# Kernel optimization log

Hardware: AMD Instinct MI355X
Metric: run time of the kernel (lower is better)

Reference implementation:

```python
import jax, jax.numpy as jnp
import numpy as np

B, T, C = 4, 2048, 1024
H = 16
HD = C // H  # 64


def setup_inputs() -> dict:
    key = jax.random.key(0)
    k1, k2, k3 = jax.random.split(key, 3)
    x = jax.random.normal(k1, (B, T, C), dtype=jnp.float32)
    # learned params (torch Linear y = x @ W.T stored here as [in, out])
    Wqkv = jax.random.normal(k2, (C, 3 * C), dtype=jnp.float32) * (C ** -0.5)
    Wout = jax.random.normal(k3, (C, C), dtype=jnp.float32) * (C ** -0.5)
    bout = jnp.zeros((C,), dtype=jnp.float32)
    causal_mask = jnp.tril(jnp.ones((1, 1, T, T), dtype=bool))
    return {"x": x, "causal_mask": causal_mask, "Wqkv": Wqkv, "Wout": Wout, "bout": bout}


def reference(x, causal_mask, Wqkv, Wout, bout):
    b, t, c = x.shape
    scale = HD ** -0.5
    qkv = x @ Wqkv  # [B,T,3C]
    q, k, v = jnp.split(qkv, 3, axis=-1)
    # [B,T,C] -> [B,H,T,hd]
    q = q.reshape(b, t, H, HD).transpose(0, 2, 1, 3)
    k = k.reshape(b, t, H, HD).transpose(0, 2, 1, 3)
    v = v.reshape(b, t, H, HD).transpose(0, 2, 1, 3)
    att = jnp.einsum("bhqd,bhkd->bhqk", q, k) * scale  # [B,H,T,T]
    att = jnp.where(causal_mask, att, -jnp.inf)
    att = jax.nn.softmax(att, axis=-1)
    # dropout in eval mode == identity
    out = jnp.einsum("bhqk,bhkd->bhqd", att, v)  # [B,H,T,hd]
    out = out.transpose(0, 2, 1, 3).reshape(b, t, c)
    return out @ Wout + bout


if __name__ == "__main__":
    inp = setup_inputs()
    y = jax.jit(reference)(**inp)
    print(y.shape, y.dtype)
```

## Files before the change

kernel.cpp:

```cpp
#include <hip/hip_runtime.h>
#include <hip/hip_bf16.h>
#include <stdint.h>


typedef __bf16 bf16;
typedef __bf16 bf16x4 __attribute__((ext_vector_type(4)));
typedef __bf16 bf16x8 __attribute__((ext_vector_type(8)));
typedef float floatx4 __attribute__((ext_vector_type(4)));

#define MFMA16(a, b, c) __builtin_amdgcn_mfma_f32_16x16x32_bf16(a, b, c, 0, 0, 0)

#if defined(__has_builtin)
#if __has_builtin(__builtin_amdgcn_global_load_lds)
#define HAS_GLL 1
#endif
#endif

#ifdef HAS_GLL
__device__ __forceinline__ void gll16(const bf16* g, bf16* l) {
  __builtin_amdgcn_global_load_lds(
      (const __attribute__((address_space(1))) unsigned int*)g,
      (__attribute__((address_space(3))) unsigned int*)l, 16, 0, 0);
}
#endif

__global__ __launch_bounds__(256)
void convert_x(const float* __restrict__ in, bf16* __restrict__ out) {
  const size_t i = (size_t)blockIdx.x * 256 + threadIdx.x;
  const float4* p = (const float4*)in + i * 2;
  float4 a = p[0], b = p[1];
  bf16x8 v;
  v[0] = (bf16)a.x; v[1] = (bf16)a.y; v[2] = (bf16)a.z; v[3] = (bf16)a.w;
  v[4] = (bf16)b.x; v[5] = (bf16)b.y; v[6] = (bf16)b.z; v[7] = (bf16)b.w;
  *((bf16x8*)out + i) = v;
}

__global__ __launch_bounds__(256)
void transpose_w(const float* __restrict__ W, bf16* __restrict__ Wt, int K, int N) {
  __shared__ bf16 tile[32][33];
  const int k0 = blockIdx.y * 32, n0 = blockIdx.x * 32;
  const int t = threadIdx.x;
  {
    const int r = t >> 3, c4 = (t & 7) * 4;
    float4 v = *(const float4*)(W + (size_t)(k0 + r) * N + n0 + c4);
    tile[r][c4 + 0] = (bf16)v.x;
    tile[r][c4 + 1] = (bf16)v.y;
    tile[r][c4 + 2] = (bf16)v.z;
    tile[r][c4 + 3] = (bf16)v.w;
  }
  __syncthreads();
  {
    const int nr = t >> 3, kc = (t & 7) * 4;
    bf16x4 o;
#pragma unroll
    for (int j = 0; j < 4; ++j) o[j] = tile[kc + j][nr];
    *(bf16x4*)(Wt + (size_t)(n0 + nr) * K + k0 + kc) = o;
  }
}

template <int MODE>
__global__ __launch_bounds__(256, 3)
void gemm_bt(const bf16* __restrict__ A, const bf16* __restrict__ Bt,
             const float* __restrict__ bias, void* __restrict__ Cv,
             bf16* __restrict__ Vout, int M, int N, int K) {
  __shared__ __align__(16) bf16 As[128 * 64];
  __shared__ __align__(16) bf16 Bs[128 * 64];

  const int t = threadIdx.x, lane = t & 63, w = t >> 6;
  const int m_ = lane & 15, quad = lane >> 4;
  const int wm = w >> 1, wn = w & 1;
  const int m0 = blockIdx.y * 128, n0 = blockIdx.x * 128;

  floatx4 acc[4][4];
#pragma unroll
  for (int i = 0; i < 4; ++i)
#pragma unroll
    for (int j = 0; j < 4; ++j) {
      floatx4 z = {0.f, 0.f, 0.f, 0.f};
      acc[i][j] = z;
    }

  for (int k0 = 0; k0 < K; k0 += 64) {
#pragma unroll
    for (int i = 0; i < 4; ++i) {
      const int R0 = i * 32 + w * 8;
      const int R = R0 + (lane >> 3);
      const int sg = (lane & 7) ^ (R & 7);
      const bf16* ga = A + (size_t)(m0 + R) * K + k0 + sg * 8;
      const bf16* gb = Bt + (size_t)(n0 + R) * K + k0 + sg * 8;
#ifdef HAS_GLL
      gll16(ga, As + (size_t)R0 * 64);
      gll16(gb, Bs + (size_t)R0 * 64);
#else
      *(bf16x8*)(As + (size_t)R * 64 + (lane & 7) * 8) = *(const bf16x8*)ga;
      *(bf16x8*)(Bs + (size_t)R * 64 + (lane & 7) * 8) = *(const bf16x8*)gb;
#endif
    }
    __syncthreads();

#pragma unroll
    for (int kc = 0; kc < 2; ++kc) {
      bf16x8 af[4], bfr[4];
#pragma unroll
      for (int mt = 0; mt < 4; ++mt) {
        const int r = wm * 64 + mt * 16 + m_;
        const int slot = ((kc << 2) | quad) ^ (r & 7);
        af[mt] = *(const bf16x8*)(As + (size_t)r * 64 + slot * 8);
      }
#pragma unroll
      for (int nt = 0; nt < 4; ++nt) {
        const int rn = wn * 64 + nt * 16 + m_;
        const int slot = ((kc << 2) | quad) ^ (rn & 7);
        bfr[nt] = *(const bf16x8*)(Bs + (size_t)rn * 64 + slot * 8);
      }
#pragma unroll
      for (int mt = 0; mt < 4; ++mt)
#pragma unroll
        for (int nt = 0; nt < 4; ++nt)
          acc[mt][nt] = MFMA16(af[mt], bfr[nt], acc[mt][nt]);
    }
    __syncthreads();
  }

  if (MODE == 0) {
#pragma unroll
    for (int mt = 0; mt < 4; ++mt)
#pragma unroll
      for (int nt = 0; nt < 4; ++nt) {
        const int col = n0 + wn * 64 + nt * 16 + m_;
        const float bv = bias[col];
#pragma unroll
        for (int r = 0; r < 4; ++r) {
          const int row = m0 + wm * 64 + mt * 16 + quad * 4 + r;
          ((float*)Cv)[(size_t)row * N + col] = acc[mt][nt][r] + bv;
        }
      }
  } else {
    if (n0 < 2048) {
      const float sc = (n0 < 1024) ? 0.18033688f : 1.0f;
#pragma unroll
      for (int mt = 0; mt < 4; ++mt)
#pragma unroll
        for (int nt = 0; nt < 4; ++nt) {
          const int col = n0 + wn * 64 + nt * 16 + m_;
#pragma unroll
          for (int r = 0; r < 4; ++r) {
            const int row = m0 + wm * 64 + mt * 16 + quad * 4 + r;
            ((bf16*)Cv)[(size_t)row * 2048 + col] = (bf16)(acc[mt][nt][r] * sc);
          }
        }
    } else {
#pragma unroll
      for (int mt = 0; mt < 4; ++mt) {
        const int rowb = m0 + wm * 64 + mt * 16 + quad * 4;
        const int bb = rowb >> 11, tok = rowb & 2047;
#pragma unroll
        for (int nt = 0; nt < 4; ++nt) {
          const int c = n0 - 2048 + wn * 64 + nt * 16 + m_;
          const int h = c >> 6, d = c & 63;
          bf16x4 pw;
#pragma unroll
          for (int r = 0; r < 4; ++r) pw[r] = (bf16)acc[mt][nt][r];
          *(bf16x4*)(Vout + ((size_t)(bb * 16 + h) * 64 + d) * 2048 + tok) = pw;
        }
      }
    }
  }
}

__global__ __launch_bounds__(256, 2)
void attn_fwd(const bf16* __restrict__ qk, const bf16* __restrict__ vtp,
              bf16* __restrict__ attnout) {
  constexpr int KS = 72;
  __shared__ __align__(16) bf16 Ks[64 * KS];
  __shared__ __align__(16) bf16 VT[64 * KS];
  __shared__ __align__(16) bf16 Pl[128 * KS];

  const int t = threadIdx.x, lane = t & 63, w = t >> 6;
  const int m_ = lane & 15, quad = lane >> 4;
  const int bh = blockIdx.x;
  const int qbmap[16] = {15, 14, 13, 12, 8, 9, 10, 11, 7, 6, 5, 4, 0, 1, 2, 3};
  const int qb = qbmap[blockIdx.y];
  const int b = bh >> 4, h = bh & 15;
  const int srcbase = (lane & 48) + ((lane & 48) >> 2);

  const bf16* Qp = qk + (size_t)b * 2048 * 2048 + h * 64;
  const bf16* Kp = qk + (size_t)b * 2048 * 2048 + 1024 + h * 64;
  const bf16* Vt = vtp + (size_t)bh * 64 * 2048;

  const int sr0 = t >> 3, sg0 = t & 7;
  const int sr1 = (t + 256) >> 3, sg1 = t & 7;

  const int q0w = qb * 128 + w * 32;

  bf16x8 qf[2][2];
#pragma unroll
  for (int mt = 0; mt < 2; ++mt)
#pragma unroll
    for (int kc = 0; kc < 2; ++kc)
      qf[mt][kc] = *(const bf16x8*)(Qp + (size_t)(q0w + mt * 16 + m_) * 2048 +
                                    kc * 32 + quad * 8);

  floatx4 o[2][4];
#pragma unroll
  for (int mt = 0; mt < 2; ++mt)
#pragma unroll
    for (int nt = 0; nt < 4; ++nt) {
      floatx4 z = {0.f, 0.f, 0.f, 0.f};
      o[mt][nt] = z;
    }
  float lrow[2] = {0.f, 0.f};

  const int nch = 2 * qb + 2;

  bf16x8 kr0, kr1, vr0, vr1;
  kr0 = *(const bf16x8*)(Kp + (size_t)sr0 * 2048 + sg0 * 8);
  kr1 = *(const bf16x8*)(Kp + (size_t)sr1 * 2048 + sg1 * 8);
  vr0 = *(const bf16x8*)(Vt + (size_t)sr0 * 2048 + sg0 * 8);
  vr1 = *(const bf16x8*)(Vt + (size_t)sr1 * 2048 + sg1 * 8);

  for (int ch = 0; ch < nch; ++ch) {
    const int kb = ch * 64;
    __syncthreads();
    *(bf16x8*)(Ks + (size_t)sr0 * KS + sg0 * 8) = kr0;
    *(bf16x8*)(Ks + (size_t)sr1 * KS + sg1 * 8) = kr1;
    *(bf16x8*)(VT + (size_t)sr0 * KS + sg0 * 8) = vr0;
    *(bf16x8*)(VT + (size_t)sr1 * KS + sg1 * 8) = vr1;
    __syncthreads();
    if (ch + 1 < nch) {
      const int kn = kb + 64;
      kr0 = *(const bf16x8*)(Kp + (size_t)(kn + sr0) * 2048 + sg0 * 8);
      kr1 = *(const bf16x8*)(Kp + (size_t)(kn + sr1) * 2048 + sg1 * 8);
      vr0 = *(const bf16x8*)(Vt + (size_t)sr0 * 2048 + kn + sg0 * 8);
      vr1 = *(const bf16x8*)(Vt + (size_t)sr1 * 2048 + kn + sg1 * 8);
    }

    if (kb <= q0w + 31) {
      bf16x8 kf[4][2];
#pragma unroll
      for (int kt = 0; kt < 4; ++kt)
#pragma unroll
        for (int kc = 0; kc < 2; ++kc)
          kf[kt][kc] = *(const bf16x8*)(Ks + (size_t)(kt * 16 + m_) * KS +
                                        kc * 32 + quad * 8);
      const bool need_mask = (kb + 63 > q0w);
#pragma unroll
      for (int mt = 0; mt < 2; ++mt) {
        floatx4 s[4];
#pragma unroll
        for (int kt = 0; kt < 4; ++kt) {
          floatx4 z = {0.f, 0.f, 0.f, 0.f};
          z = MFMA16(kf[kt][0], qf[mt][0], z);
          z = MFMA16(kf[kt][1], qf[mt][1], z);
          s[kt] = z;
        }
        if (need_mask) {
          const int qglob = q0w + mt * 16 + m_;
#pragma unroll
          for (int kt = 0; kt < 4; ++kt)
#pragma unroll
            for (int r = 0; r < 4; ++r)
              if (kb + kt * 16 + quad * 4 + r > qglob) s[kt][r] = -1e30f;
        }
        float psum = 0.f;
#pragma unroll
        for (int kt = 0; kt < 4; ++kt) {
          bf16x4 pw;
#pragma unroll
          for (int r = 0; r < 4; ++r) {
            const float p = exp2f(s[kt][r]);
            psum += p;
            pw[r] = (bf16)p;
          }
          *(bf16x4*)(Pl + (size_t)((w * 2 + mt) * 16 + m_) * KS + kt * 16 +
                     quad * 4) = pw;
        }
        lrow[mt] += psum;
      }
      bf16x8 vf[4][2];
#pragma unroll
      for (int nt = 0; nt < 4; ++nt)
#pragma unroll
        for (int kc = 0; kc < 2; ++kc)
          vf[nt][kc] = *(const bf16x8*)(VT + (size_t)(nt * 16 + m_) * KS +
                                        kc * 32 + quad * 8);
#pragma unroll
      for (int mt = 0; mt < 2; ++mt) {
        const bf16* prow = Pl + (size_t)((w * 2 + mt) * 16 + m_) * KS;
        const bf16x8 pf0 = *(const bf16x8*)(prow + quad * 8);
        const bf16x8 pf1 = *(const bf16x8*)(prow + 32 + quad * 8);
#pragma unroll
        for (int nt = 0; nt < 4; ++nt) {
          o[mt][nt] = MFMA16(pf0, vf[nt][0], o[mt][nt]);
          o[mt][nt] = MFMA16(pf1, vf[nt][1], o[mt][nt]);
        }
      }
    }
  }

#pragma unroll
  for (int mt = 0; mt < 2; ++mt) {
    float l = lrow[mt];
    l += __shfl_xor(l, 16);
    l += __shfl_xor(l, 32);
    const float linv = 1.0f / l;
#pragma unroll
    for (int r = 0; r < 4; ++r) {
      const float inv = __shfl(linv, srcbase + r);
      const int row = q0w + mt * 16 + quad * 4 + r;
      const size_t orow = ((size_t)b * 2048 + row) * 1024 + h * 64;
#pragma unroll
      for (int nt = 0; nt < 4; ++nt)
        attnout[orow + nt * 16 + m_] = (bf16)(o[mt][nt][r] * inv);
    }
  }
}

extern "C" void kernel_launch(void* const* d_in, const int* in_sizes, int n_in,
                              void* d_out, int out_size, void* d_ws, size_t ws_size,
                              hipStream_t stream) {
  (void)in_sizes; (void)n_in; (void)out_size; (void)ws_size;
  const float* x    = (const float*)d_in[0];
  const float* Wqkv = (const float*)d_in[2];
  const float* Wout = (const float*)d_in[3];
  const float* bout = (const float*)d_in[4];
  float* out = (float*)d_out;

  bf16* qk      = (bf16*)d_ws;
  bf16* vtp     = (bf16*)((char*)d_ws + (size_t)32 * 1024 * 1024);
  bf16* attnout = (bf16*)((char*)d_ws + (size_t)48 * 1024 * 1024);
  bf16* Wout_t  = (bf16*)d_ws;
  bf16* xbf    = (bf16*)d_out;
  bf16* Wqkv_t = (bf16*)d_out + (size_t)8192 * 1024;

  convert_x<<<4096, 256, 0, stream>>>(x, xbf);
  transpose_w<<<dim3(96, 32), 256, 0, stream>>>(Wqkv, Wqkv_t, 1024, 3072);

  gemm_bt<1><<<dim3(24, 64), 256, 0, stream>>>(xbf, Wqkv_t, nullptr, qk, vtp,
                                               8192, 3072, 1024);
  attn_fwd<<<dim3(64, 16), 256, 0, stream>>>(qk, vtp, attnout);

  transpose_w<<<dim3(32, 32), 256, 0, stream>>>(Wout, Wout_t, 1024, 1024);
  gemm_bt<0><<<dim3(8, 64), 256, 0, stream>>>(attnout, Wout_t, bout, out,
                                              nullptr, 8192, 1024, 1024);
}
```

Before: 265.1 us.

## Rewrite attention inner loop with 32x32 MFMA, register-resident P, and double-buffered LDS

```diff
diff --git a/kernel.cpp b/kernel.cpp
--- a/kernel.cpp
+++ b/kernel.cpp
@@ -7,8 +7,11 @@
 typedef __bf16 bf16x4 __attribute__((ext_vector_type(4)));
 typedef __bf16 bf16x8 __attribute__((ext_vector_type(8)));
 typedef float floatx4 __attribute__((ext_vector_type(4)));
+typedef float floatx16 __attribute__((ext_vector_type(16)));
+typedef unsigned int uintx4 __attribute__((ext_vector_type(4)));
 
 #define MFMA16(a, b, c) __builtin_amdgcn_mfma_f32_16x16x32_bf16(a, b, c, 0, 0, 0)
+#define MFMA32(a, b, c) __builtin_amdgcn_mfma_f32_32x32x16_bf16(a, b, c, 0, 0, 0)
 
 #if defined(__has_builtin)
 #if __has_builtin(__builtin_amdgcn_global_load_lds)
@@ -23,6 +26,15 @@
       (__attribute__((address_space(3))) unsigned int*)l, 16, 0, 0);
 }
 #endif
+
+__device__ __forceinline__ unsigned cvtpk(float lo, float hi) {
+  unsigned r;
+  asm("v_cvt_pk_bf16_f32 %0, %1, %2" : "=v"(r) : "v"(lo), "v"(hi));
+  return r;
+}
+__device__ __forceinline__ void pl32swap(unsigned& a, unsigned& b) {
+  asm volatile("v_permlane32_swap_b32 %0, %1" : "+v"(a), "+v"(b));
+}
 
 __global__ __launch_bounds__(256)
 void convert_x(const float* __restrict__ in, bf16* __restrict__ out) {
@@ -168,150 +180,145 @@
   }
 }
 
+__device__ __forceinline__ void stage64(const bf16* base, bf16* lds,
+                                        int lane, int w) {
+#pragma unroll
+  for (int i = 0; i < 2; ++i) {
+    const int seg = w * 2 + i;
+    const int row = seg * 8 + (lane >> 3);
+    const int g = (lane & 7) ^ (row & 7);
+#ifdef HAS_GLL
+    gll16(base + (size_t)row * 2048 + g * 8, lds + seg * 512);
+#else
+    *(bf16x8*)(lds + row * 64 + (lane & 7) * 8) =
+        *(const bf16x8*)(base + (size_t)row * 2048 + g * 8);
+#endif
+  }
+}
+
 __global__ __launch_bounds__(256, 2)
 void attn_fwd(const bf16* __restrict__ qk, const bf16* __restrict__ vtp,
               bf16* __restrict__ attnout) {
-  constexpr int KS = 72;
-  __shared__ __align__(16) bf16 Ks[64 * KS];
-  __shared__ __align__(16) bf16 VT[64 * KS];
-  __shared__ __align__(16) bf16 Pl[128 * KS];
+  __shared__ __align__(16) bf16 KsB[2][64 * 64];
+  __shared__ __align__(16) bf16 VTB[2][64 * 64];
+  __shared__ __align__(16) float Lbuf[4][32];
 
   const int t = threadIdx.x, lane = t & 63, w = t >> 6;
-  const int m_ = lane & 15, quad = lane >> 4;
+  const int ln = lane & 31, hi = lane >> 5;
   const int bh = blockIdx.x;
   const int qbmap[16] = {15, 14, 13, 12, 8, 9, 10, 11, 7, 6, 5, 4, 0, 1, 2, 3};
   const int qb = qbmap[blockIdx.y];
   const int b = bh >> 4, h = bh & 15;
-  const int srcbase = (lane & 48) + ((lane & 48) >> 2);
 
   const bf16* Qp = qk + (size_t)b * 2048 * 2048 + h * 64;
   const bf16* Kp = qk + (size_t)b * 2048 * 2048 + 1024 + h * 64;
   const bf16* Vt = vtp + (size_t)bh * 64 * 2048;
 
-  const int sr0 = t >> 3, sg0 = t & 7;
-  const int sr1 = (t + 256) >> 3, sg1 = t & 7;
-
   const int q0w = qb * 128 + w * 32;
 
-  bf16x8 qf[2][2];
-#pragma unroll
-  for (int mt = 0; mt < 2; ++mt)
-#pragma unroll
-    for (int kc = 0; kc < 2; ++kc)
-      qf[mt][kc] = *(const bf16x8*)(Qp + (size_t)(q0w + mt * 16 + m_) * 2048 +
-                                    kc * 32 + quad * 8);
-
-  floatx4 o[2][4];
-#pragma unroll
-  for (int mt = 0; mt < 2; ++mt)
-#pragma unroll
-    for (int nt = 0; nt < 4; ++nt) {
-      floatx4 z = {0.f, 0.f, 0.f, 0.f};
-      o[mt][nt] = z;
-    }
-  float lrow[2] = {0.f, 0.f};
+  bf16x8 qf[4];
+#pragma unroll
+  for (int st = 0; st < 4; ++st)
+    qf[st] = *(const bf16x8*)(Qp + (size_t)(q0w + ln) * 2048 + st * 16 + hi * 8);
+
+  floatx16 o[2];
+#pragma unroll
+  for (int nt = 0; nt < 2; ++nt)
+#pragma unroll
+    for (int r = 0; r < 16; ++r) o[nt][r] = 0.f;
+  float lrow = 0.f;
 
   const int nch = 2 * qb + 2;
 
-  bf16x8 kr0, kr1, vr0, vr1;
-  kr0 = *(const bf16x8*)(Kp + (size_t)sr0 * 2048 + sg0 * 8);
-  kr1 = *(const bf16x8*)(Kp + (size_t)sr1 * 2048 + sg1 * 8);
-  vr0 = *(const bf16x8*)(Vt + (size_t)sr0 * 2048 + sg0 * 8);
-  vr1 = *(const bf16x8*)(Vt + (size_t)sr1 * 2048 + sg1 * 8);
+  stage64(Kp, KsB[0], lane, w);
+  stage64(Vt, VTB[0], lane, w);
 
   for (int ch = 0; ch < nch; ++ch) {
     const int kb = ch * 64;
-    __syncthreads();
-    *(bf16x8*)(Ks + (size_t)sr0 * KS + sg0 * 8) = kr0;
-    *(bf16x8*)(Ks + (size_t)sr1 * KS + sg1 * 8) = kr1;
-    *(bf16x8*)(VT + (size_t)sr0 * KS + sg0 * 8) = vr0;
-    *(bf16x8*)(VT + (size_t)sr1 * KS + sg1 * 8) = vr1;
+    const int cur = ch & 1;
     __syncthreads();
     if (ch + 1 < nch) {
-      const int kn = kb + 64;
-      kr0 = *(const bf16x8*)(Kp + (size_t)(kn + sr0) * 2048 + sg0 * 8);
-      kr1 = *(const bf16x8*)(Kp + (size_t)(kn + sr1) * 2048 + sg1 * 8);
-      vr0 = *(const bf16x8*)(Vt + (size_t)sr0 * 2048 + kn + sg0 * 8);
-      vr1 = *(const bf16x8*)(Vt + (size_t)sr1 * 2048 + kn + sg1 * 8);
-    }
-
-    if (kb <= q0w + 31) {
-      bf16x8 kf[4][2];
-#pragma unroll
-      for (int kt = 0; kt < 4; ++kt)
-#pragma unroll
-        for (int kc = 0; kc < 2; ++kc)
-          kf[kt][kc] = *(const bf16x8*)(Ks + (size_t)(kt * 16 + m_) * KS +
-                                        kc * 32 + quad * 8);
-      const bool need_mask = (kb + 63 > q0w);
-#pragma unroll
-      for (int mt = 0; mt < 2; ++mt) {
-        floatx4 s[4];
-#pragma unroll
-        for (int kt = 0; kt < 4; ++kt) {
-          floatx4 z = {0.f, 0.f, 0.f, 0.f};
-          z = MFMA16(kf[kt][0], qf[mt][0], z);
-          z = MFMA16(kf[kt][1], qf[mt][1], z);
-          s[kt] = z;
-        }
+      stage64(Kp + (size_t)(kb + 64) * 2048, KsB[cur ^ 1], lane, w);
+      stage64(Vt + kb + 64, VTB[cur ^ 1], lane, w);
+    }
+    if (kb > q0w + 31) continue;
+    const bf16* Kb = KsB[cur];
+    const bf16* Vb = VTB[cur];
+    const bool need_mask = (kb + 63 > q0w);
+
+#pragma unroll
+    for (int kt = 0; kt < 2; ++kt) {
+      if (kb + kt * 32 <= q0w + 31) {
+        floatx16 s;
+#pragma unroll
+        for (int r = 0; r < 16; ++r) s[r] = 0.f;
+        const int krow = kt * 32 + ln;
+        __builtin_amdgcn_s_setprio(1);
+#pragma unroll
+        for (int st = 0; st < 4; ++st) {
+          const bf16x8 kf = *(const bf16x8*)(
+              Kb + krow * 64 + ((((st << 1) | hi) ^ (krow & 7)) << 3));
+          s = MFMA32(kf, qf[st], s);
+        }
+        __builtin_amdgcn_s_setprio(0);
         if (need_mask) {
-          const int qglob = q0w + mt * 16 + m_;
-#pragma unroll
-          for (int kt = 0; kt < 4; ++kt)
-#pragma unroll
-            for (int r = 0; r < 4; ++r)
-              if (kb + kt * 16 + quad * 4 + r > qglob) s[kt][r] = -1e30f;
-        }
+          const int qg = q0w + ln;
+          const int kbase = kb + kt * 32 + 4 * hi;
+#pragma unroll
+          for (int rq = 0; rq < 4; ++rq)
+#pragma unroll
+            for (int j = 0; j < 4; ++j)
+              if (kbase + 8 * rq + j > qg) s[rq * 4 + j] = -1e30f;
+        }
+        float p[16];
         float psum = 0.f;
 #pragma unroll
-        for (int kt = 0; kt < 4; ++kt) {
-          bf16x4 pw;
-#pragma unroll
-          for (int r = 0; r < 4; ++r) {
-            const float p = exp2f(s[kt][r]);
-            psum += p;
-            pw[r] = (bf16)p;
+        for (int r = 0; r < 16; ++r) {
+          p[r] = exp2f(s[r]);
+          psum += p[r];
+        }
+        lrow += psum;
+#pragma unroll
+        for (int sb = 0; sb < 2; ++sb) {
+          unsigned A0 = cvtpk(p[8 * sb + 0], p[8 * sb + 1]);
+          unsigned A1 = cvtpk(p[8 * sb + 2], p[8 * sb + 3]);
+          unsigned B0 = cvtpk(p[8 * sb + 4], p[8 * sb + 5]);
+          unsigned B1 = cvtpk(p[8 * sb + 6], p[8 * sb + 7]);
+          pl32swap(A0, B0);
+          pl32swap(A1, B1);
+          uintx4 fw;
+          fw[0] = A0; fw[1] = A1; fw[2] = B0; fw[3] = B1;
+          const bf16x8 paf = __builtin_bit_cast(bf16x8, fw);
+          const int st = kt * 2 + sb;
+          __builtin_amdgcn_s_setprio(1);
+#pragma unroll
+          for (int nt = 0; nt < 2; ++nt) {
+            const int vrow = nt * 32 + ln;
+            const bf16x8 vf = *(const bf16x8*)(
+                Vb + vrow * 64 + ((((st << 1) | hi) ^ (vrow & 7)) << 3));
+            o[nt] = MFMA32(paf, vf, o[nt]);
           }
-          *(bf16x4*)(Pl + (size_t)((w * 2 + mt) * 16 + m_) * KS + kt * 16 +
-                     quad * 4) = pw;
-        }
-        lrow[mt] += psum;
-      }
-      bf16x8 vf[4][2];
-#pragma unroll
-      for (int nt = 0; nt < 4; ++nt)
-#pragma unroll
-        for (int kc = 0; kc < 2; ++kc)
-          vf[nt][kc] = *(const bf16x8*)(VT + (size_t)(nt * 16 + m_) * KS +
-                                        kc * 32 + quad * 8);
-#pragma unroll
-      for (int mt = 0; mt < 2; ++mt) {
-        const bf16* prow = Pl + (size_t)((w * 2 + mt) * 16 + m_) * KS;
-        const bf16x8 pf0 = *(const bf16x8*)(prow + quad * 8);
-        const bf16x8 pf1 = *(const bf16x8*)(prow + 32 + quad * 8);
-#pragma unroll
-        for (int nt = 0; nt < 4; ++nt) {
-          o[mt][nt] = MFMA16(pf0, vf[nt][0], o[mt][nt]);
-          o[mt][nt] = MFMA16(pf1, vf[nt][1], o[mt][nt]);
-        }
-      }
-    }
-  }
-
-#pragma unroll
-  for (int mt = 0; mt < 2; ++mt) {
-    float l = lrow[mt];
-    l += __shfl_xor(l, 16);
-    l += __shfl_xor(l, 32);
-    const float linv = 1.0f / l;
-#pragma unroll
-    for (int r = 0; r < 4; ++r) {
-      const float inv = __shfl(linv, srcbase + r);
-      const int row = q0w + mt * 16 + quad * 4 + r;
-      const size_t orow = ((size_t)b * 2048 + row) * 1024 + h * 64;
-#pragma unroll
-      for (int nt = 0; nt < 4; ++nt)
-        attnout[orow + nt * 16 + m_] = (bf16)(o[mt][nt][r] * inv);
+          __builtin_amdgcn_s_setprio(0);
+        }
+      }
+    }
+  }
+
+  const float lt = lrow + __shfl_xor(lrow, 32);
+  if (hi == 0) Lbuf[w][ln] = 1.0f / lt;
+  __syncthreads();
+
+#pragma unroll
+  for (int nt = 0; nt < 2; ++nt) {
+#pragma unroll
+    for (int rq = 0; rq < 4; ++rq) {
+      const floatx4 lv = *(const floatx4*)&Lbuf[w][8 * rq + 4 * hi];
+#pragma unroll
+      for (int j = 0; j < 4; ++j) {
+        const int row = q0w + 8 * rq + 4 * hi + j;
+        attnout[((size_t)b * 2048 + row) * 1024 + h * 64 + nt * 32 + ln] =
+            (bf16)(o[nt][rq * 4 + j] * lv[j]);
+      }
     }
   }
 }
```

Result: faster. 258.5 us (-2.5%).
